# Kernel tuning notes

Measured on AMD Instinct MI355X. Metric: run time of the kernel, lower is better.

## Reference

```python
import jax, jax.numpy as jnp
import numpy as np

B, S, H = 16, 4, 1024
NH, CACHE, HD = 16, 8192, 64


def setup_inputs() -> dict:
    key = jax.random.key(0)
    ks = jax.random.split(key, 7)
    return {
        "x": jax.random.normal(ks[0], (B, S, H), dtype=jnp.float32),
        "k_cache": jax.random.normal(ks[1], (B, NH, CACHE, HD), dtype=jnp.float32),
        "v_cache": jax.random.normal(ks[2], (B, NH, CACHE, HD), dtype=jnp.float32),
        "W_in": jax.random.normal(ks[3], (H, 3 * H), dtype=jnp.float32) * 0.02,
        "b_in": jnp.zeros((3 * H,), dtype=jnp.float32),
        "W_out": jax.random.normal(ks[4], (H, H), dtype=jnp.float32) * 0.02,
        "b_out": jnp.zeros((H,), dtype=jnp.float32),
    }


def reference(x, k_cache, v_cache, W_in, b_in, W_out, b_out):
    b, s, h = x.shape
    nh, hd = k_cache.shape[1], k_cache.shape[3]
    qkv = x @ W_in + b_in                          # [b, s, 3h]
    q, k, v = jnp.split(qkv, 3, axis=-1)
    # [b, s, h] -> [b, nh, s, hd]
    q = q.reshape(b, s, nh, hd).transpose(0, 2, 1, 3)
    k = k.reshape(b, s, nh, hd).transpose(0, 2, 1, 3)
    v = v.reshape(b, s, nh, hd).transpose(0, 2, 1, 3)
    # naive cache growth via concat (faithful to torch.cat baseline)
    k = jnp.concatenate([k_cache, k], axis=2)      # [b, nh, cache+s, hd]
    v = jnp.concatenate([v_cache, v], axis=2)
    scale = 1.0 / jnp.sqrt(jnp.float32(hd))
    scores = jnp.einsum("bhqd,bhkd->bhqk", q, k) * scale
    attn = jax.nn.softmax(scores, axis=-1)
    out = jnp.einsum("bhqk,bhkd->bhqd", attn, v)   # [b, nh, s, hd]
    out = out.transpose(0, 2, 1, 3).reshape(b, s, h)
    out = out @ W_out + b_out
    return out, k, v
```

## Files before the change

kernel.cpp:

```cpp
#include <hip/hip_runtime.h>
#include <math.h>

#define NHEAD 16
#define HDIM 64
#define BATCH 16
#define SEQ 4
#define CACHE_LEN 8192
#define TOT_LEN 8196
#define S_STRIDE 8200

typedef float f4 __attribute__((ext_vector_type(4)));

__device__ __forceinline__ float row16_reduce(float x) {
    int t;
    t = __builtin_amdgcn_update_dpp(0, __float_as_int(x), 0xB1, 0xF, 0xF, true);
    x += __int_as_float(t);
    t = __builtin_amdgcn_update_dpp(0, __float_as_int(x), 0x4E, 0xF, 0xF, true);
    x += __int_as_float(t);
    t = __builtin_amdgcn_update_dpp(0, __float_as_int(x), 0x124, 0xF, 0xF, true);
    x += __int_as_float(t);
    t = __builtin_amdgcn_update_dpp(0, __float_as_int(x), 0x128, 0xF, 0xF, true);
    x += __int_as_float(t);
    return x;
}

template <int N>
__global__ __launch_bounds__(256) void gemm64(const float* __restrict__ x,
                                              const float* __restrict__ W,
                                              const float* __restrict__ bias,
                                              float* __restrict__ out) {
    __shared__ float xs[8][1024];
    __shared__ float red[4][8][64];
    const int tid = threadIdx.x;
    const int colBase = blockIdx.x * 64;
    const int rowBase = blockIdx.y * 8;
    for (int idx = tid; idx < 8 * 1024; idx += 256) {
        xs[idx >> 10][idx & 1023] = x[(size_t)(rowBase + (idx >> 10)) * 1024 + (idx & 1023)];
    }
    __syncthreads();
    const int col = tid & 63;
    const int kseg = tid >> 6;
    float acc[8] = {0.f, 0.f, 0.f, 0.f, 0.f, 0.f, 0.f, 0.f};
    const float* Wp = W + (size_t)colBase + col;
    const int k0 = kseg * 256;
#pragma unroll 4
    for (int k = k0; k < k0 + 256; ++k) {
        const float w = Wp[(size_t)k * N];
#pragma unroll
        for (int r = 0; r < 8; ++r) acc[r] += xs[r][k] * w;
    }
#pragma unroll
    for (int r = 0; r < 8; ++r) red[kseg][r][col] = acc[r];
    __syncthreads();
    if (kseg == 0) {
        const float bv = bias[colBase + col];
#pragma unroll
        for (int r = 0; r < 8; ++r) {
            out[(size_t)(rowBase + r) * N + colBase + col] =
                red[0][r][col] + red[1][r][col] + red[2][r][col] + red[3][r][col] + bv;
        }
    }
}

__global__ __launch_bounds__(1024) void k_pass(const float* __restrict__ k_cache,
                                               const float* __restrict__ qkv,
                                               float* __restrict__ k_out,
                                               f4* __restrict__ s_ws,
                                               float* __restrict__ ml_ws) {
    const int bh = blockIdx.x;
    const int b = bh >> 4;
    const int h = bh & 15;
    const int tid = threadIdx.x;
    const int slot = tid >> 4;
    const int quad = tid & 15;

    float q[4][4];
#pragma unroll
    for (int qs = 0; qs < 4; ++qs) {
        const f4 qv = *reinterpret_cast<const f4*>(
            qkv + (size_t)(b * SEQ + qs) * 3072 + h * HDIM + quad * 4);
        q[qs][0] = qv.x * 0.125f;
        q[qs][1] = qv.y * 0.125f;
        q[qs][2] = qv.z * 0.125f;
        q[qs][3] = qv.w * 0.125f;
    }

    const f4* kc = reinterpret_cast<const f4*>(k_cache + (size_t)bh * CACHE_LEN * HDIM);
    f4* ko = reinterpret_cast<f4*>(k_out + (size_t)bh * TOT_LEN * HDIM);
    f4* sb = s_ws + (size_t)bh * S_STRIDE;

    float m[4], l[4];
#pragma unroll
    for (int qs = 0; qs < 4; ++qs) {
        m[qs] = -INFINITY;
        l[qs] = 0.f;
    }

    for (int g = 0; g < CACHE_LEN / 256; ++g) {
        f4 kk[4];
        int fi[4];
#pragma unroll
        for (int j = 0; j < 4; ++j) {
            const int key = g * 256 + j * 64 + slot;
            fi[j] = key * 16 + quad;
            kk[j] = __builtin_nontemporal_load(kc + fi[j]);
        }
#pragma unroll
        for (int j = 0; j < 4; ++j) __builtin_nontemporal_store(kk[j], ko + fi[j]);

        float s[4][4];
#pragma unroll
        for (int j = 0; j < 4; ++j) {
#pragma unroll
            for (int qs = 0; qs < 4; ++qs) {
                float d = q[qs][0] * kk[j].x + q[qs][1] * kk[j].y + q[qs][2] * kk[j].z +
                          q[qs][3] * kk[j].w;
                s[j][qs] = row16_reduce(d);
            }
        }
#pragma unroll
        for (int qs = 0; qs < 4; ++qs) {
            const float tmax = fmaxf(fmaxf(s[0][qs], s[1][qs]), fmaxf(s[2][qs], s[3][qs]));
            const float mn = fmaxf(m[qs], tmax);
            const float corr = __expf(m[qs] - mn);
            m[qs] = mn;
            l[qs] = l[qs] * corr + ((__expf(s[0][qs] - mn) + __expf(s[1][qs] - mn)) +
                                    (__expf(s[2][qs] - mn) + __expf(s[3][qs] - mn)));
        }
        if (quad == 0) {
#pragma unroll
            for (int j = 0; j < 4; ++j) {
                __builtin_nontemporal_store((f4){s[j][0], s[j][1], s[j][2], s[j][3]},
                                            sb + g * 256 + j * 64 + slot);
            }
        }
    }

    if (slot < 4) {
        const int key = CACHE_LEN + slot;
        const f4 k4 = *reinterpret_cast<const f4*>(
            qkv + (size_t)(b * SEQ + slot) * 3072 + 1024 + h * HDIM + quad * 4);
        ko[key * 16 + quad] = k4;
        float s[4];
#pragma unroll
        for (int qs = 0; qs < 4; ++qs) {
            float d = q[qs][0] * k4.x + q[qs][1] * k4.y + q[qs][2] * k4.z + q[qs][3] * k4.w;
            s[qs] = row16_reduce(d);
        }
#pragma unroll
        for (int qs = 0; qs < 4; ++qs) {
            const float mn = fmaxf(m[qs], s[qs]);
            const float corr = __expf(m[qs] - mn);
            m[qs] = mn;
            l[qs] = l[qs] * corr + __expf(s[qs] - mn);
        }
        if (quad == 0) sb[CACHE_LEN + slot] = (f4){s[0], s[1], s[2], s[3]};
    }

    __shared__ float rm[64][4];
    __shared__ float rl[64][4];
    if (quad == 0) {
#pragma unroll
        for (int qs = 0; qs < 4; ++qs) {
            rm[slot][qs] = m[qs];
            rl[slot][qs] = l[qs];
        }
    }
    __syncthreads();
    if (tid < 4) {
        float M = -INFINITY;
        for (int s2 = 0; s2 < 64; ++s2) M = fmaxf(M, rm[s2][tid]);
        float L = 0.f;
        for (int s2 = 0; s2 < 64; ++s2) L += rl[s2][tid] * __expf(rm[s2][tid] - M);
        ml_ws[bh * 8 + tid] = M;
        ml_ws[bh * 8 + 4 + tid] = L;
    }
}

__global__ __launch_bounds__(1024) void v_pass(const float* __restrict__ v_cache,
                                               const float* __restrict__ qkv,
                                               const float* __restrict__ ml_ws,
                                               const f4* __restrict__ s_ws,
                                               float* __restrict__ v_out,
                                               float* __restrict__ attn_out) {
    const int bh = blockIdx.x;
    const int b = bh >> 4;
    const int h = bh & 15;
    const int tid = threadIdx.x;
    const int slot = tid >> 4;
    const int quad = tid & 15;

    float m[4], linv[4];
#pragma unroll
    for (int qs = 0; qs < 4; ++qs) {
        m[qs] = ml_ws[bh * 8 + qs];
        linv[qs] = 1.0f / ml_ws[bh * 8 + 4 + qs];
    }

    const f4* vc = reinterpret_cast<const f4*>(v_cache + (size_t)bh * CACHE_LEN * HDIM);
    f4* vo = reinterpret_cast<f4*>(v_out + (size_t)bh * TOT_LEN * HDIM);
    const f4* sb = s_ws + (size_t)bh * S_STRIDE;

    float acc[4][4];
#pragma unroll
    for (int qs = 0; qs < 4; ++qs) acc[qs][0] = acc[qs][1] = acc[qs][2] = acc[qs][3] = 0.f;

    for (int g = 0; g < CACHE_LEN / 256; ++g) {
        f4 vv[4], s4[4];
        int fi[4];
#pragma unroll
        for (int j = 0; j < 4; ++j) {
            const int key = g * 256 + j * 64 + slot;
            fi[j] = key * 16 + quad;
            vv[j] = __builtin_nontemporal_load(vc + fi[j]);
        }
#pragma unroll
        for (int j = 0; j < 4; ++j) s4[j] = __builtin_nontemporal_load(sb + g * 256 + j * 64 + slot);
#pragma unroll
        for (int j = 0; j < 4; ++j) __builtin_nontemporal_store(vv[j], vo + fi[j]);
#pragma unroll
        for (int j = 0; j < 4; ++j) {
#pragma unroll
            for (int qs = 0; qs < 4; ++qs) {
                const float w = __expf(s4[j][qs] - m[qs]);
                acc[qs][0] += w * vv[j].x;
                acc[qs][1] += w * vv[j].y;
                acc[qs][2] += w * vv[j].z;
                acc[qs][3] += w * vv[j].w;
            }
        }
    }

    if (slot < 4) {
        const int key = CACHE_LEN + slot;
        const f4 v4 = *reinterpret_cast<const f4*>(
            qkv + (size_t)(b * SEQ + slot) * 3072 + 2048 + h * HDIM + quad * 4);
        vo[key * 16 + quad] = v4;
        const f4 s4 = sb[CACHE_LEN + slot];
#pragma unroll
        for (int qs = 0; qs < 4; ++qs) {
            const float w = __expf(s4[qs] - m[qs]);
            acc[qs][0] += w * v4.x;
            acc[qs][1] += w * v4.y;
            acc[qs][2] += w * v4.z;
            acc[qs][3] += w * v4.w;
        }
    }

    __shared__ float red_acc[64][64];
    __shared__ float red_part[4][64];
    for (int qs = 0; qs < 4; ++qs) {
        __syncthreads();
        *reinterpret_cast<f4*>(&red_acc[slot][quad * 4]) =
            (f4){acc[qs][0], acc[qs][1], acc[qs][2], acc[qs][3]};
        __syncthreads();
        if (tid < 256) {
            const int dim = tid & 63;
            const int part = tid >> 6;
            float sum = 0.f;
            for (int s2 = 0; s2 < 16; ++s2) sum += red_acc[part * 16 + s2][dim];
            red_part[part][dim] = sum;
        }
        __syncthreads();
        if (tid < 64) {
            const float sum =
                red_part[0][tid] + red_part[1][tid] + red_part[2][tid] + red_part[3][tid];
            attn_out[(size_t)(b * SEQ + qs) * 1024 + h * HDIM + tid] = sum * linv[qs];
        }
    }
}

extern "C" void kernel_launch(void* const* d_in, const int* in_sizes, int n_in,
                              void* d_out, int out_size, void* d_ws, size_t ws_size,
                              hipStream_t stream) {
    const float* x       = (const float*)d_in[0];
    const float* k_cache = (const float*)d_in[1];
    const float* v_cache = (const float*)d_in[2];
    const float* W_in    = (const float*)d_in[3];
    const float* b_in    = (const float*)d_in[4];
    const float* W_out   = (const float*)d_in[5];
    const float* b_out   = (const float*)d_in[6];

    float* out   = (float*)d_out;
    float* k_out = out + (size_t)BATCH * SEQ * 1024;
    float* v_out = k_out + (size_t)BATCH * NHEAD * TOT_LEN * HDIM;

    float* ws_qkv  = (float*)d_ws;
    float* ws_attn = ws_qkv + 64 * 3072;
    float* ml_ws   = ws_attn + 64 * 1024;
    f4*    s_ws    = (f4*)(ml_ws + 256 * 8);

    gemm64<3072><<<dim3(48, 8), 256, 0, stream>>>(x, W_in, b_in, ws_qkv);
    k_pass<<<dim3(256), 1024, 0, stream>>>(k_cache, ws_qkv, k_out, s_ws, ml_ws);
    v_pass<<<dim3(256), 1024, 0, stream>>>(v_cache, ws_qkv, ml_ws, s_ws, v_out, ws_attn);
    gemm64<1024><<<dim3(16, 8), 256, 0, stream>>>(ws_attn, W_out, b_out, out);
}
```

Baseline: 466.5 us.

## Split KV sequence into four partitions per head with partial softmax merge

The K and V passes now launch four 256-thread blocks per (batch, head), each covering 2048 keys, instead of one 1024-thread block per head. Per-partition max and sum statistics are merged at the start of the V pass. Per-partition attention outputs are summed while the output GEMM loads its input tile. Nontemporal stores are also replaced with regular stores. The aim is more, smaller blocks for better CU occupancy and scheduling on a bandwidth-bound copy-plus-attention workload, at the cost of extra workspace traffic and a cross-partition reduction.

```diff
diff --git a/kernel.cpp b/kernel.cpp
--- a/kernel.cpp
+++ b/kernel.cpp
@@ -8,6 +8,8 @@
 #define CACHE_LEN 8192
 #define TOT_LEN 8196
 #define S_STRIDE 8200
+#define PARTS 4
+#define PKEYS 2048
 
 typedef float f4 __attribute__((ext_vector_type(4)));
 
@@ -24,11 +26,10 @@
     return x;
 }
 
-template <int N>
-__global__ __launch_bounds__(256) void gemm64(const float* __restrict__ x,
-                                              const float* __restrict__ W,
-                                              const float* __restrict__ bias,
-                                              float* __restrict__ out) {
+__global__ __launch_bounds__(256) void gemm_qkv(const float* __restrict__ x,
+                                                const float* __restrict__ W,
+                                                const float* __restrict__ bias,
+                                                float* __restrict__ out) {
     __shared__ float xs[8][1024];
     __shared__ float red[4][8][64];
     const int tid = threadIdx.x;
@@ -45,7 +46,7 @@
     const int k0 = kseg * 256;
 #pragma unroll 4
     for (int k = k0; k < k0 + 256; ++k) {
-        const float w = Wp[(size_t)k * N];
+        const float w = Wp[(size_t)k * 3072];
 #pragma unroll
         for (int r = 0; r < 8; ++r) acc[r] += xs[r][k] * w;
     }
@@ -56,18 +57,20 @@
         const float bv = bias[colBase + col];
 #pragma unroll
         for (int r = 0; r < 8; ++r) {
-            out[(size_t)(rowBase + r) * N + colBase + col] =
+            out[(size_t)(rowBase + r) * 3072 + colBase + col] =
                 red[0][r][col] + red[1][r][col] + red[2][r][col] + red[3][r][col] + bv;
         }
     }
 }
 
-__global__ __launch_bounds__(1024) void k_pass(const float* __restrict__ k_cache,
-                                               const float* __restrict__ qkv,
-                                               float* __restrict__ k_out,
-                                               f4* __restrict__ s_ws,
-                                               float* __restrict__ ml_ws) {
-    const int bh = blockIdx.x;
+__global__ __launch_bounds__(256) void k_pass(const float* __restrict__ k_cache,
+                                              const float* __restrict__ qkv,
+                                              float* __restrict__ k_out,
+                                              f4* __restrict__ s_ws,
+                                              float* __restrict__ ml_ws) {
+    const int bid = blockIdx.x;
+    const int bh = bid >> 2;
+    const int part = bid & 3;
     const int b = bh >> 4;
     const int h = bh & 15;
     const int tid = threadIdx.x;
@@ -88,6 +91,7 @@
     const f4* kc = reinterpret_cast<const f4*>(k_cache + (size_t)bh * CACHE_LEN * HDIM);
     f4* ko = reinterpret_cast<f4*>(k_out + (size_t)bh * TOT_LEN * HDIM);
     f4* sb = s_ws + (size_t)bh * S_STRIDE;
+    const int kbase = part * PKEYS;
 
     float m[4], l[4];
 #pragma unroll
@@ -96,17 +100,16 @@
         l[qs] = 0.f;
     }
 
-    for (int g = 0; g < CACHE_LEN / 256; ++g) {
+    for (int g = 0; g < PKEYS / 64; ++g) {
         f4 kk[4];
-        int fi[4];
+        int key[4];
 #pragma unroll
         for (int j = 0; j < 4; ++j) {
-            const int key = g * 256 + j * 64 + slot;
-            fi[j] = key * 16 + quad;
-            kk[j] = __builtin_nontemporal_load(kc + fi[j]);
-        }
-#pragma unroll
-        for (int j = 0; j < 4; ++j) __builtin_nontemporal_store(kk[j], ko + fi[j]);
+            key[j] = kbase + g * 64 + j * 16 + slot;
+            kk[j] = __builtin_nontemporal_load(kc + key[j] * 16 + quad);
+        }
+#pragma unroll
+        for (int j = 0; j < 4; ++j) ko[key[j] * 16 + quad] = kk[j];
 
         float s[4][4];
 #pragma unroll
@@ -129,14 +132,11 @@
         }
         if (quad == 0) {
 #pragma unroll
-            for (int j = 0; j < 4; ++j) {
-                __builtin_nontemporal_store((f4){s[j][0], s[j][1], s[j][2], s[j][3]},
-                                            sb + g * 256 + j * 64 + slot);
-            }
-        }
-    }
-
-    if (slot < 4) {
+            for (int j = 0; j < 4; ++j) sb[key[j]] = (f4){s[j][0], s[j][1], s[j][2], s[j][3]};
+        }
+    }
+
+    if (part == 3 && slot < 4) {
         const int key = CACHE_LEN + slot;
         const f4 k4 = *reinterpret_cast<const f4*>(
             qkv + (size_t)(b * SEQ + slot) * 3072 + 1024 + h * HDIM + quad * 4);
@@ -154,11 +154,11 @@
             m[qs] = mn;
             l[qs] = l[qs] * corr + __expf(s[qs] - mn);
         }
-        if (quad == 0) sb[CACHE_LEN + slot] = (f4){s[0], s[1], s[2], s[3]};
-    }
-
-    __shared__ float rm[64][4];
-    __shared__ float rl[64][4];
+        if (quad == 0) sb[key] = (f4){s[0], s[1], s[2], s[3]};
+    }
+
+    __shared__ float rm[16][4];
+    __shared__ float rl[16][4];
     if (quad == 0) {
 #pragma unroll
         for (int qs = 0; qs < 4; ++qs) {
@@ -169,103 +169,164 @@
     __syncthreads();
     if (tid < 4) {
         float M = -INFINITY;
-        for (int s2 = 0; s2 < 64; ++s2) M = fmaxf(M, rm[s2][tid]);
+        for (int s2 = 0; s2 < 16; ++s2) M = fmaxf(M, rm[s2][tid]);
         float L = 0.f;
-        for (int s2 = 0; s2 < 64; ++s2) L += rl[s2][tid] * __expf(rm[s2][tid] - M);
-        ml_ws[bh * 8 + tid] = M;
-        ml_ws[bh * 8 + 4 + tid] = L;
-    }
-}
-
-__global__ __launch_bounds__(1024) void v_pass(const float* __restrict__ v_cache,
-                                               const float* __restrict__ qkv,
-                                               const float* __restrict__ ml_ws,
-                                               const f4* __restrict__ s_ws,
-                                               float* __restrict__ v_out,
-                                               float* __restrict__ attn_out) {
-    const int bh = blockIdx.x;
+        for (int s2 = 0; s2 < 16; ++s2) L += rl[s2][tid] * __expf(rm[s2][tid] - M);
+        ml_ws[bid * 8 + tid] = M;
+        ml_ws[bid * 8 + 4 + tid] = L;
+    }
+}
+
+__global__ __launch_bounds__(256) void v_pass(const float* __restrict__ v_cache,
+                                              const float* __restrict__ qkv,
+                                              const float* __restrict__ ml_ws,
+                                              const f4* __restrict__ s_ws,
+                                              float* __restrict__ v_out,
+                                              float* __restrict__ pacc) {
+    const int bid = blockIdx.x;
+    const int bh = bid >> 2;
+    const int part = bid & 3;
     const int b = bh >> 4;
     const int h = bh & 15;
     const int tid = threadIdx.x;
     const int slot = tid >> 4;
     const int quad = tid & 15;
 
-    float m[4], linv[4];
-#pragma unroll
-    for (int qs = 0; qs < 4; ++qs) {
-        m[qs] = ml_ws[bh * 8 + qs];
-        linv[qs] = 1.0f / ml_ws[bh * 8 + 4 + qs];
-    }
+    __shared__ float sm_M[4];
+    __shared__ float sm_Li[4];
+    if (tid < 4) {
+        float M = -INFINITY;
+#pragma unroll
+        for (int p = 0; p < 4; ++p) M = fmaxf(M, ml_ws[(bh * 4 + p) * 8 + tid]);
+        float L = 0.f;
+#pragma unroll
+        for (int p = 0; p < 4; ++p) {
+            L += ml_ws[(bh * 4 + p) * 8 + 4 + tid] *
+                 __expf(ml_ws[(bh * 4 + p) * 8 + tid] - M);
+        }
+        sm_M[tid] = M;
+        sm_Li[tid] = 1.0f / L;
+    }
+    __syncthreads();
+    const float m0 = sm_M[0], m1 = sm_M[1], m2 = sm_M[2], m3 = sm_M[3];
 
     const f4* vc = reinterpret_cast<const f4*>(v_cache + (size_t)bh * CACHE_LEN * HDIM);
     f4* vo = reinterpret_cast<f4*>(v_out + (size_t)bh * TOT_LEN * HDIM);
     const f4* sb = s_ws + (size_t)bh * S_STRIDE;
+    const int kbase = part * PKEYS;
 
     float acc[4][4];
 #pragma unroll
     for (int qs = 0; qs < 4; ++qs) acc[qs][0] = acc[qs][1] = acc[qs][2] = acc[qs][3] = 0.f;
 
-    for (int g = 0; g < CACHE_LEN / 256; ++g) {
+    for (int g = 0; g < PKEYS / 64; ++g) {
         f4 vv[4], s4[4];
-        int fi[4];
+        int key[4];
 #pragma unroll
         for (int j = 0; j < 4; ++j) {
-            const int key = g * 256 + j * 64 + slot;
-            fi[j] = key * 16 + quad;
-            vv[j] = __builtin_nontemporal_load(vc + fi[j]);
-        }
-#pragma unroll
-        for (int j = 0; j < 4; ++j) s4[j] = __builtin_nontemporal_load(sb + g * 256 + j * 64 + slot);
-#pragma unroll
-        for (int j = 0; j < 4; ++j) __builtin_nontemporal_store(vv[j], vo + fi[j]);
+            key[j] = kbase + g * 64 + j * 16 + slot;
+            vv[j] = __builtin_nontemporal_load(vc + key[j] * 16 + quad);
+        }
+#pragma unroll
+        for (int j = 0; j < 4; ++j) s4[j] = sb[key[j]];
+#pragma unroll
+        for (int j = 0; j < 4; ++j) vo[key[j] * 16 + quad] = vv[j];
 #pragma unroll
         for (int j = 0; j < 4; ++j) {
-#pragma unroll
-            for (int qs = 0; qs < 4; ++qs) {
-                const float w = __expf(s4[j][qs] - m[qs]);
-                acc[qs][0] += w * vv[j].x;
-                acc[qs][1] += w * vv[j].y;
-                acc[qs][2] += w * vv[j].z;
-                acc[qs][3] += w * vv[j].w;
-            }
-        }
-    }
-
-    if (slot < 4) {
+            const float w0 = __expf(s4[j].x - m0);
+            const float w1 = __expf(s4[j].y - m1);
+            const float w2 = __expf(s4[j].z - m2);
+            const float w3 = __expf(s4[j].w - m3);
+            acc[0][0] += w0 * vv[j].x; acc[0][1] += w0 * vv[j].y;
+            acc[0][2] += w0 * vv[j].z; acc[0][3] += w0 * vv[j].w;
+            acc[1][0] += w1 * vv[j].x; acc[1][1] += w1 * vv[j].y;
+            acc[1][2] += w1 * vv[j].z; acc[1][3] += w1 * vv[j].w;
+            acc[2][0] += w2 * vv[j].x; acc[2][1] += w2 * vv[j].y;
+            acc[2][2] += w2 * vv[j].z; acc[2][3] += w2 * vv[j].w;
+            acc[3][0] += w3 * vv[j].x; acc[3][1] += w3 * vv[j].y;
+            acc[3][2] += w3 * vv[j].z; acc[3][3] += w3 * vv[j].w;
+        }
+    }
+
+    if (part == 3 && slot < 4) {
         const int key = CACHE_LEN + slot;
         const f4 v4 = *reinterpret_cast<const f4*>(
             qkv + (size_t)(b * SEQ + slot) * 3072 + 2048 + h * HDIM + quad * 4);
         vo[key * 16 + quad] = v4;
-        const f4 s4 = sb[CACHE_LEN + slot];
-#pragma unroll
-        for (int qs = 0; qs < 4; ++qs) {
-            const float w = __expf(s4[qs] - m[qs]);
-            acc[qs][0] += w * v4.x;
-            acc[qs][1] += w * v4.y;
-            acc[qs][2] += w * v4.z;
-            acc[qs][3] += w * v4.w;
-        }
-    }
-
-    __shared__ float red_acc[64][64];
+        const f4 s4 = sb[key];
+        const float w0 = __expf(s4.x - m0);
+        const float w1 = __expf(s4.y - m1);
+        const float w2 = __expf(s4.z - m2);
+        const float w3 = __expf(s4.w - m3);
+        acc[0][0] += w0 * v4.x; acc[0][1] += w0 * v4.y; acc[0][2] += w0 * v4.z; acc[0][3] += w0 * v4.w;
+        acc[1][0] += w1 * v4.x; acc[1][1] += w1 * v4.y; acc[1][2] += w1 * v4.z; acc[1][3] += w1 * v4.w;
+        acc[2][0] += w2 * v4.x; acc[2][1] += w2 * v4.y; acc[2][2] += w2 * v4.z; acc[2][3] += w2 * v4.w;
+        acc[3][0] += w3 * v4.x; acc[3][1] += w3 * v4.y; acc[3][2] += w3 * v4.z; acc[3][3] += w3 * v4.w;
+    }
+
+    __shared__ float red_acc[16][64];
     __shared__ float red_part[4][64];
     for (int qs = 0; qs < 4; ++qs) {
         __syncthreads();
         *reinterpret_cast<f4*>(&red_acc[slot][quad * 4]) =
             (f4){acc[qs][0], acc[qs][1], acc[qs][2], acc[qs][3]};
         __syncthreads();
-        if (tid < 256) {
+        {
             const int dim = tid & 63;
-            const int part = tid >> 6;
+            const int sg = tid >> 6;
             float sum = 0.f;
-            for (int s2 = 0; s2 < 16; ++s2) sum += red_acc[part * 16 + s2][dim];
-            red_part[part][dim] = sum;
+#pragma unroll
+            for (int s2 = 0; s2 < 4; ++s2) sum += red_acc[sg * 4 + s2][dim];
+            red_part[sg][dim] = sum;
         }
         __syncthreads();
         if (tid < 64) {
             const float sum =
                 red_part[0][tid] + red_part[1][tid] + red_part[2][tid] + red_part[3][tid];
-            attn_out[(size_t)(b * SEQ + qs) * 1024 + h * HDIM + tid] = sum * linv[qs];
+            pacc[((size_t)bid * 4 + qs) * 64 + tid] = sum * sm_Li[qs];
+        }
+    }
+}
+
+__global__ __launch_bounds__(256) void gemm_out(const float* __restrict__ pacc,
+                                                const float* __restrict__ W,
+                                                const float* __restrict__ bias,
+                                                float* __restrict__ out) {
+    __shared__ float xs[8][1024];
+    __shared__ float red[4][8][64];
+    const int tid = threadIdx.x;
+    const int colBase = blockIdx.x * 64;
+    const int rowBase = blockIdx.y * 8;
+    for (int idx = tid; idx < 8 * 1024; idx += 256) {
+        const int r = idx >> 10;
+        const int c = idx & 1023;
+        const int row = rowBase + r;
+        const int b = row >> 2, qs = row & 3;
+        const int h = c >> 6, d = c & 63;
+        const size_t base = ((size_t)(b * 16 + h) * 4) * 4 * 64 + qs * 64 + d;
+        xs[r][c] = pacc[base] + pacc[base + 256] + pacc[base + 512] + pacc[base + 768];
+    }
+    __syncthreads();
+    const int col = tid & 63;
+    const int kseg = tid >> 6;
+    float acc[8] = {0.f, 0.f, 0.f, 0.f, 0.f, 0.f, 0.f, 0.f};
+    const float* Wp = W + (size_t)colBase + col;
+    const int k0 = kseg * 256;
+#pragma unroll 4
+    for (int k = k0; k < k0 + 256; ++k) {
+        const float w = Wp[(size_t)k * 1024];
+#pragma unroll
+        for (int r = 0; r < 8; ++r) acc[r] += xs[r][k] * w;
+    }
+#pragma unroll
+    for (int r = 0; r < 8; ++r) red[kseg][r][col] = acc[r];
+    __syncthreads();
+    if (kseg == 0) {
+        const float bv = bias[colBase + col];
+#pragma unroll
+        for (int r = 0; r < 8; ++r) {
+            out[(size_t)(rowBase + r) * 1024 + colBase + col] =
+                red[0][r][col] + red[1][r][col] + red[2][r][col] + red[3][r][col] + bv;
         }
     }
 }
@@ -285,13 +346,13 @@
     float* k_out = out + (size_t)BATCH * SEQ * 1024;
     float* v_out = k_out + (size_t)BATCH * NHEAD * TOT_LEN * HDIM;
 
-    float* ws_qkv  = (float*)d_ws;
-    float* ws_attn = ws_qkv + 64 * 3072;
-    float* ml_ws   = ws_attn + 64 * 1024;
-    f4*    s_ws    = (f4*)(ml_ws + 256 * 8);
-
-    gemm64<3072><<<dim3(48, 8), 256, 0, stream>>>(x, W_in, b_in, ws_qkv);
-    k_pass<<<dim3(256), 1024, 0, stream>>>(k_cache, ws_qkv, k_out, s_ws, ml_ws);
-    v_pass<<<dim3(256), 1024, 0, stream>>>(v_cache, ws_qkv, ml_ws, s_ws, v_out, ws_attn);
-    gemm64<1024><<<dim3(16, 8), 256, 0, stream>>>(ws_attn, W_out, b_out, out);
-}
+    float* ws_qkv = (float*)d_ws;
+    float* ml_ws  = ws_qkv + 64 * 3072;
+    float* pacc   = ml_ws + 1024 * 8;
+    f4*    s_ws   = (f4*)(pacc + 1024 * 4 * 64);
+
+    gemm_qkv<<<dim3(48, 8), 256, 0, stream>>>(x, W_in, b_in, ws_qkv);
+    k_pass<<<dim3(1024), 256, 0, stream>>>(k_cache, ws_qkv, k_out, s_ws, ml_ws);
+    v_pass<<<dim3(1024), 256, 0, stream>>>(v_cache, ws_qkv, ml_ws, s_ws, v_out, pacc);
+    gemm_out<<<dim3(16, 8), 256, 0, stream>>>(pacc, W_out, b_out, out);
+}
```

Result: slower. 542.1 us (+16.2%).
